# Kernel optimization log

Measured on AMD Instinct MI355X. Metric: run time of the kernel, lower is better.

The kernel has to match this reference:

```python
import math
import jax, jax.numpy as jnp
from jax import lax
import numpy as np

C, H, W, N, K = 256, 64, 64, 16, 7

def setup_inputs() -> dict:
    key = jax.random.key(0)
    k0, k1, k2, k3, k4 = jax.random.split(key, 5)
    x = jax.random.normal(k0, (N, C, H, W), dtype=jnp.float32)
    p_2_w = 0.02 * jax.random.normal(k1, (1, C, H, 1), dtype=jnp.float32)
    # nn.Conv2d(c, c, (1,5), groups=1, bias=False) -> weight [c, c, 1, 5]
    fan_in = C * 1 * 5
    bound = 1.0 / math.sqrt(fan_in)
    p_3_w = jax.random.uniform(k2, (C, C, 1, 5), dtype=jnp.float32, minval=-bound, maxval=bound)
    p_4_w = 0.02 * jax.random.normal(k3, (1, C, K, 1, 1), dtype=jnp.float32)
    p_6_w = jax.random.uniform(k4, (K, 1), dtype=jnp.float32, minval=-7.0, maxval=7.0)
    return {"x": x, "p_2_w": p_2_w, "p_3_w": p_3_w, "p_4_w": p_4_w, "p_6_w": p_6_w}

def reference(x, p_2_w, p_3_w, p_4_w, p_6_w):
    n, c, h, w = x.shape
    k = p_4_w.shape[2]  # 7 taps
    pad = (k - 1) // 2
    # F.unfold with kernel (1,7), pad (0,3): stack 7 width-shifted copies -> [n,c,7,h,w]
    xp = jnp.pad(x, ((0, 0), (0, 0), (0, 0), (pad, pad)))
    t_1 = jnp.stack([xp[..., i:i + w] for i in range(k)], axis=2)
    # per-(channel,row) scaling then dense 1x5 conv
    t_2 = p_2_w * x
    t_3 = lax.conv_general_dilated(
        t_2, p_3_w, window_strides=(1, 1), padding=[(0, 0), (2, 2)],
        dimension_numbers=("NCHW", "OIHW", "NCHW"))
    # weighted tap-sum: (p_4_w * t_1) contracted over taps with p_6_w[:,0]
    t_4 = p_4_w * t_1
    t_6 = jnp.einsum("nckhw,kf->ncfhw", t_4, p_6_w)[:, :, 0]  # [n,c,h,w]
    t_5 = jax.nn.relu(x)
    s = h * w
    # channel-attention matrix [n,c,c]
    t_7 = jnp.einsum("ncs,nds->ncd", t_3.reshape(n, c, s), t_6.reshape(n, c, s))
    t_7 = t_7 * (1.0 / math.sqrt(s))
    # bmm(t_5^T, t_7) -> [n,s,d]; permuting to [n,d,h,w] == einsum 'ncs,ncd->nds'
    out = jnp.einsum("ncs,ncd->nds", t_5.reshape(n, c, s), t_7)
    out = out * (1.0 / math.sqrt(c))
    return out.reshape(n, c, h, w)
```

## Files before the change

kernel.cpp:

```cpp
#include <hip/hip_runtime.h>
#include <hip/hip_bf16.h>

typedef __attribute__((ext_vector_type(8))) short bf16x8;
typedef __attribute__((ext_vector_type(4))) float f32x4;

#define NB 16
#define CD 256
#define HD 64
#define WD 64
#define WP 68
#define SD 4096
#define KU 1280

__device__ __forceinline__ void gload16(const void* g, void* lds) {
  __builtin_amdgcn_global_load_lds(
      (const __attribute__((address_space(1))) unsigned int*)g,
      (__attribute__((address_space(3))) unsigned int*)lds, 16, 0, 0);
}

__global__ __launch_bounds__(256) void prep_x(const float* __restrict__ x,
                                              const float* __restrict__ p2,
                                              const float* __restrict__ p4,
                                              const float* __restrict__ p6,
                                              const float* __restrict__ p3,
                                              __hip_bfloat16* __restrict__ t2p,
                                              __hip_bfloat16* __restrict__ t5T,
                                              __hip_bfloat16* __restrict__ t6,
                                              __hip_bfloat16* __restrict__ A) {
  int h = blockIdx.x;
  int cb = blockIdx.y;
  int n = blockIdx.z;
  int c0 = cb * 64;
  __shared__ float xwp[64][72];
  __shared__ __hip_bfloat16 t5l[64][72];
  __shared__ __hip_bfloat16 t2l[64][72];
  int t = threadIdx.x;

  {
    int bid = (n * 64 + h) * 4 + cb;
    int id = bid * 256 + t;
    if (id < CD * KU) {
      int o = id / KU;
      int r = id - o * KU;
      int j = r >> 8;
      int c = r & 255;
      A[id] = __float2bfloat16(p3[(o * CD + c) * 5 + j]);
    }
  }

  {
    int r = t >> 2, cc = t & 3;
    xwp[r][cc] = 0.f;
    xwp[r][68 + cc] = 0.f;
  }

  {
    int w = t & 63, cg = (t >> 6) * 16;
    __hip_bfloat16 o5[16], o2[16];
#pragma unroll
    for (int j = 0; j < 16; ++j) {
      int c = c0 + cg + j;
      float xv = x[(((size_t)n * CD + c) * HD + h) * WD + w];
      float sc = p2[c * HD + h];
      xwp[cg + j][4 + w] = xv;
      o5[j] = __float2bfloat16(fmaxf(xv, 0.f));
      o2[j] = __float2bfloat16(sc * xv);
    }
    *reinterpret_cast<bf16x8*>(&t5l[w][cg]) = *reinterpret_cast<const bf16x8*>(&o5[0]);
    *reinterpret_cast<bf16x8*>(&t5l[w][cg + 8]) = *reinterpret_cast<const bf16x8*>(&o5[8]);
    *reinterpret_cast<bf16x8*>(&t2l[w][cg]) = *reinterpret_cast<const bf16x8*>(&o2[0]);
    *reinterpret_cast<bf16x8*>(&t2l[w][cg + 8]) = *reinterpret_cast<const bf16x8*>(&o2[8]);
  }
  __syncthreads();

  __hip_bfloat16* t2pn = t2p + (size_t)n * HD * WP * CD;

  {
    int ws = t >> 2, ch = (t & 3) * 16;
    bf16x8 v0 = *reinterpret_cast<const bf16x8*>(&t5l[ws][ch]);
    bf16x8 v1 = *reinterpret_cast<const bf16x8*>(&t5l[ws][ch + 8]);
    size_t s = (size_t)h * 64 + ws;
    *reinterpret_cast<bf16x8*>(&t5T[((size_t)n * SD + s) * CD + c0 + ch]) = v0;
    *reinterpret_cast<bf16x8*>(&t5T[((size_t)n * SD + s) * CD + c0 + ch + 8]) = v1;
    bf16x8 u0 = *reinterpret_cast<const bf16x8*>(&t2l[ws][ch]);
    bf16x8 u1 = *reinterpret_cast<const bf16x8*>(&t2l[ws][ch + 8]);
    *reinterpret_cast<bf16x8*>(&t2pn[((size_t)h * WP + ws + 2) * CD + c0 + ch]) = u0;
    *reinterpret_cast<bf16x8*>(&t2pn[((size_t)h * WP + ws + 2) * CD + c0 + ch + 8]) = u1;
  }
  if (t < 32) {
    int pi = t >> 3;
    int wp = (pi < 2) ? pi : pi + 64;
    int cc = (t & 7) * 8;
    bf16x8 z = (bf16x8){0, 0, 0, 0, 0, 0, 0, 0};
    *reinterpret_cast<bf16x8*>(&t2pn[((size_t)h * WP + wp) * CD + c0 + cc]) = z;
  }

  {
    int cl = t >> 2, w16 = (t & 3) * 16;
    float hx[24];
#pragma unroll
    for (int q = 0; q < 6; ++q) {
      float4 v = *reinterpret_cast<const float4*>(&xwp[cl][w16 + q * 4]);
      hx[q * 4 + 0] = v.x;
      hx[q * 4 + 1] = v.y;
      hx[q * 4 + 2] = v.z;
      hx[q * 4 + 3] = v.w;
    }
    float wt[7];
#pragma unroll
    for (int k = 0; k < 7; ++k) wt[k] = p4[(c0 + cl) * 7 + k] * p6[k];
    __hip_bfloat16 o6[16];
#pragma unroll
    for (int u = 0; u < 16; ++u) {
      float acc = 0.f;
#pragma unroll
      for (int k = 0; k < 7; ++k) acc += wt[k] * hx[u + 1 + k];
      o6[u] = __float2bfloat16(acc);
    }
    size_t base = ((size_t)n * CD + c0 + cl) * SD + h * 64 + w16;
    *reinterpret_cast<bf16x8*>(&t6[base]) = *reinterpret_cast<const bf16x8*>(&o6[0]);
    *reinterpret_cast<bf16x8*>(&t6[base + 8]) = *reinterpret_cast<const bf16x8*>(&o6[8]);
  }
}

#define VMWAIT(N) asm volatile("s_waitcnt vmcnt(" #N ")" ::: "memory")
#define BARRIER() __builtin_amdgcn_s_barrier()

#define ST4(kt, bi)                                                                    \
  do {                                                                                 \
    char* dst = lb + ((bi) << 15) + t * 16;                                            \
    gload16(gA0 + (kt) * 64, dst);                                                     \
    gload16(gA1 + (kt) * 64, dst + 8192);                                              \
    gload16(gB0 + (kt) * 64, dst + 16384);                                             \
    gload16(gB1 + (kt) * 64, dst + 24576);                                             \
  } while (0)

#define LDF(bi, AV, BV)                                                                \
  do {                                                                                 \
    const char* ba = lb + ((bi) << 15);                                                \
    _Pragma("unroll") for (int mf = 0; mf < 8; ++mf) {                                 \
      int row = wm * 128 + mf * 16 + l16;                                              \
      AV[mf] = *reinterpret_cast<const bf16x8*>(ba + row * 64 + ((lg ^ rxor) * 16));   \
    }                                                                                  \
    _Pragma("unroll") for (int nf = 0; nf < 4; ++nf) {                                 \
      int row = wn * 64 + nf * 16 + l16;                                               \
      BV[nf] = *reinterpret_cast<const bf16x8*>(ba + 16384 + row * 64 +                \
                                                ((lg ^ rxor) * 16));                   \
    }                                                                                  \
  } while (0)

#define MM(AV, BV)                                                                     \
  do {                                                                                 \
    __builtin_amdgcn_s_setprio(1);                                                     \
    _Pragma("unroll") for (int mf = 0; mf < 8; ++mf)                                   \
        _Pragma("unroll") for (int nf = 0; nf < 4; ++nf)                               \
            acc[mf][nf] = __builtin_amdgcn_mfma_f32_16x16x32_bf16(AV[mf], BV[nf],      \
                                                                  acc[mf][nf], 0, 0, 0); \
    __builtin_amdgcn_s_setprio(0);                                                     \
  } while (0)

__global__ __launch_bounds__(512, 2) void gemm_b8(const __hip_bfloat16* __restrict__ A,
                                                  const __hip_bfloat16* __restrict__ t2p,
                                                  __hip_bfloat16* __restrict__ t3) {
  __shared__ __align__(16) __hip_bfloat16 lds[65536];
  char* lb = (char*)lds;
  const int n = blockIdx.z;
  const int sb = blockIdx.x;
  const int t = threadIdx.x;
  const int wv = t >> 6, lane = t & 63;
  const int wm = wv >> 2, wn = wv & 3;
  const int l16 = lane & 15, lg = lane >> 4;
  const int s0 = sb * 256;
  const int rxor = (l16 >> 1) & 3;
  const char* Ab = (const char*)A;
  const char* t2pb = (const char*)(t2p + (size_t)n * HD * WP * CD);
  const int cbsrc = ((t & 3) ^ ((t >> 3) & 3)) * 16;

  const int r0 = t >> 2;
  const char* gA0 = Ab + (size_t)r0 * 2560 + cbsrc;
  const char* gA1 = Ab + (size_t)(r0 + 128) * 2560 + cbsrc;
  const int s1 = s0 + r0, s2 = s0 + r0 + 128;
  const char* gB0 = t2pb + (size_t)(s1 + 4 * (s1 >> 6)) * 512 + cbsrc;
  const char* gB1 = t2pb + (size_t)(s2 + 4 * (s2 >> 6)) * 512 + cbsrc;

  f32x4 acc[8][4];
#pragma unroll
  for (int i = 0; i < 8; ++i)
#pragma unroll
    for (int j = 0; j < 4; ++j) acc[i][j] = (f32x4){0.f, 0.f, 0.f, 0.f};

  bf16x8 avX[8], bvX[4], avY[8], bvY[4];

  ST4(0, 0);
  ST4(1, 1);
  VMWAIT(4);
  BARRIER();
  LDF(0, avX, bvX);

  for (int k2 = 0; k2 < 18; ++k2) {
    const int kt = k2 * 2;
    ST4(kt + 2, (kt + 2) & 3);
    MM(avX, bvX);
    VMWAIT(4);
    BARRIER();
    LDF((kt + 1) & 3, avY, bvY);
    ST4(kt + 3, (kt + 3) & 3);
    MM(avY, bvY);
    VMWAIT(4);
    BARRIER();
    LDF((kt + 2) & 3, avX, bvX);
  }
  ST4(38, 2);
  MM(avX, bvX);
  VMWAIT(4);
  BARRIER();
  LDF(1, avY, bvY);
  ST4(39, 3);
  MM(avY, bvY);
  VMWAIT(4);
  BARRIER();
  LDF(2, avX, bvX);
  MM(avX, bvX);
  VMWAIT(0);
  BARRIER();
  LDF(3, avY, bvY);
  MM(avY, bvY);

  __hip_bfloat16* t3n = t3 + (size_t)n * CD * SD;
#pragma unroll
  for (int im = 0; im < 8; ++im)
#pragma unroll
    for (int in = 0; in < 4; ++in) {
      int row0 = wm * 128 + im * 16 + lg * 4;
      int col = s0 + wn * 64 + in * 16 + l16;
#pragma unroll
      for (int r = 0; r < 4; ++r)
        t3n[(size_t)(row0 + r) * SD + col] = __float2bfloat16(acc[im][in][r]);
    }
}

__global__ __launch_bounds__(256) void gemm_c_part(const __hip_bfloat16* __restrict__ t6,
                                                   const __hip_bfloat16* __restrict__ t3,
                                                   float* __restrict__ P4) {
  __shared__ __align__(16) __hip_bfloat16 lA[64 * 64];
  __shared__ __align__(16) __hip_bfloat16 lB[64 * 64];
  int bx = blockIdx.x;
  int cbk = bx & 3, kc = bx >> 2;
  int db = blockIdx.y;
  int n = blockIdx.z;
  int t = threadIdx.x;
  int wave = t >> 6, lane = t & 63;
  int wm = wave >> 1, wn = wave & 1;
  int l16 = lane & 15, lg = lane >> 4;
  int d0 = db * 64;
  int c0 = cbk * 64;
  int kbase = kc * 1024;
  const __hip_bfloat16* An = t6 + (size_t)n * CD * SD + kbase;
  const __hip_bfloat16* Bn = t3 + (size_t)n * CD * SD + kbase;

  int srow = t >> 3;
  int scol = (t & 7) * 8;
  const __hip_bfloat16* gA0 = An + (size_t)(d0 + srow) * SD + scol;
  const __hip_bfloat16* gA1 = An + (size_t)(d0 + srow + 32) * SD + scol;
  const __hip_bfloat16* gB0 = Bn + (size_t)(c0 + srow) * SD + scol;
  const __hip_bfloat16* gB1 = Bn + (size_t)(c0 + srow + 32) * SD + scol;
  __hip_bfloat16* lAd0 = &lA[t * 8];
  __hip_bfloat16* lAd1 = &lA[t * 8 + 32 * 64];
  __hip_bfloat16* lBd0 = &lB[t * 8];
  __hip_bfloat16* lBd1 = &lB[t * 8 + 32 * 64];

  f32x4 acc[2][2];
#pragma unroll
  for (int mi = 0; mi < 2; ++mi)
#pragma unroll
    for (int ni = 0; ni < 2; ++ni) acc[mi][ni] = (f32x4){0.f, 0.f, 0.f, 0.f};

  gload16(gA0, lAd0);
  gload16(gA1, lAd1);
  gload16(gB0, lBd0);
  gload16(gB1, lBd1);

  for (int k = 0; k < 16; ++k) {
    __syncthreads();
#pragma unroll
    for (int ks = 0; ks < 2; ++ks) {
      bf16x8 a[2], b[2];
#pragma unroll
      for (int mi = 0; mi < 2; ++mi)
        a[mi] = *reinterpret_cast<const bf16x8*>(&lA[(wm * 32 + mi * 16 + l16) * 64 + ks * 32 + lg * 8]);
#pragma unroll
      for (int ni = 0; ni < 2; ++ni)
        b[ni] = *reinterpret_cast<const bf16x8*>(&lB[(wn * 32 + ni * 16 + l16) * 64 + ks * 32 + lg * 8]);
#pragma unroll
      for (int mi = 0; mi < 2; ++mi)
#pragma unroll
        for (int ni = 0; ni < 2; ++ni)
          acc[mi][ni] = __builtin_amdgcn_mfma_f32_16x16x32_bf16(a[mi], b[ni], acc[mi][ni], 0, 0, 0);
    }
    __syncthreads();
    if (k < 15) {
      int kk = (k + 1) * 64;
      gload16(gA0 + kk, lAd0);
      gload16(gA1 + kk, lAd1);
      gload16(gB0 + kk, lBd0);
      gload16(gB1 + kk, lBd1);
    }
  }

  float* Pn = P4 + ((size_t)kc * NB + n) * CD * CD;
#pragma unroll
  for (int mi = 0; mi < 2; ++mi)
#pragma unroll
    for (int ni = 0; ni < 2; ++ni) {
      int col = c0 + wn * 32 + ni * 16 + l16;
      int row0 = d0 + wm * 32 + mi * 16 + lg * 4;
#pragma unroll
      for (int r = 0; r < 4; ++r)
        Pn[(size_t)(row0 + r) * CD + col] = acc[mi][ni][r];
    }
}

__global__ __launch_bounds__(256) void reduce_P(const float* __restrict__ P4,
                                                __hip_bfloat16* __restrict__ P) {
  size_t i = ((size_t)blockIdx.x * 256 + threadIdx.x) * 4;
  const size_t stride = (size_t)NB * CD * CD;
  float4 a = *reinterpret_cast<const float4*>(P4 + i);
  float4 b = *reinterpret_cast<const float4*>(P4 + stride + i);
  float4 c = *reinterpret_cast<const float4*>(P4 + 2 * stride + i);
  float4 d = *reinterpret_cast<const float4*>(P4 + 3 * stride + i);
  __hip_bfloat16 o[4];
  o[0] = __float2bfloat16((a.x + b.x + c.x + d.x) * 0.015625f);
  o[1] = __float2bfloat16((a.y + b.y + c.y + d.y) * 0.015625f);
  o[2] = __float2bfloat16((a.z + b.z + c.z + d.z) * 0.015625f);
  o[3] = __float2bfloat16((a.w + b.w + c.w + d.w) * 0.015625f);
  *reinterpret_cast<short4*>(&P[i]) = *reinterpret_cast<const short4*>(o);
}

#define DSTAGE_A(i, kk)                                                                \
  gload16(Pb + (size_t)((i) * 32 + wv4 * 8 + (lane >> 3)) * 512 + (kk) * 128 + cbsrc,  \
          (char*)lA + (i) * 4096 + wv4 * 1024)
#define DSTAGE_B(i, kk)                                                                \
  gload16(Tb + (size_t)(s0 + (i) * 32 + wv4 * 8 + (lane >> 3)) * 512 + (kk) * 128 + cbsrc, \
          (char*)lB + (i) * 4096 + wv4 * 1024)

__global__ __launch_bounds__(256, 2) void gemm_d(const __hip_bfloat16* __restrict__ P,
                                                 const __hip_bfloat16* __restrict__ t5T,
                                                 float* __restrict__ out) {
  __shared__ __align__(16) __hip_bfloat16 lA[256 * 64];
  __shared__ __align__(16) __hip_bfloat16 lB[128 * 64];
  const int n = blockIdx.z;
  const int sb = blockIdx.x;
  const int t = threadIdx.x;
  const int wv4 = t >> 6, lane = t & 63;
  const int wm = wv4 >> 1, wn = wv4 & 1;
  const int l16 = lane & 15, lg = lane >> 4;
  const int s0 = sb * 128;
  const char* Pb = (const char*)(P + (size_t)n * CD * CD);
  const char* Tb = (const char*)(t5T + (size_t)n * SD * CD);
  const int cbsrc = ((lane & 7) ^ (lane >> 3)) * 16;
  const int lxor = (l16 & 7) * 8;

  f32x4 acc[8][4];
#pragma unroll
  for (int i = 0; i < 8; ++i)
#pragma unroll
    for (int j = 0; j < 4; ++j) acc[i][j] = (f32x4){0.f, 0.f, 0.f, 0.f};

#pragma unroll
  for (int i = 0; i < 8; ++i) DSTAGE_A(i, 0);
#pragma unroll
  for (int i = 0; i < 4; ++i) DSTAGE_B(i, 0);

  for (int k = 0; k < 4; ++k) {
    __syncthreads();
#pragma unroll
    for (int ks = 0; ks < 2; ++ks) {
      int cb = (ks * 32 + lg * 8) ^ lxor;
      bf16x8 a[8], b[4];
#pragma unroll
      for (int mf = 0; mf < 8; ++mf)
        a[mf] = *reinterpret_cast<const bf16x8*>(&lA[(wm * 128 + mf * 16 + l16) * 64 + cb]);
#pragma unroll
      for (int nf = 0; nf < 4; ++nf)
        b[nf] = *reinterpret_cast<const bf16x8*>(&lB[(wn * 64 + nf * 16 + l16) * 64 + cb]);
#pragma unroll
      for (int mf = 0; mf < 8; ++mf)
#pragma unroll
        for (int nf = 0; nf < 4; ++nf)
          acc[mf][nf] = __builtin_amdgcn_mfma_f32_16x16x32_bf16(a[mf], b[nf], acc[mf][nf], 0, 0, 0);
    }
    __syncthreads();
    if (k < 3) {
      int kk = k + 1;
#pragma unroll
      for (int i = 0; i < 8; ++i) DSTAGE_A(i, kk);
#pragma unroll
      for (int i = 0; i < 4; ++i) DSTAGE_B(i, kk);
    }
  }

  float* outn = out + (size_t)n * CD * SD;
#pragma unroll
  for (int mf = 0; mf < 8; ++mf)
#pragma unroll
    for (int nf = 0; nf < 4; ++nf) {
      int col = s0 + wn * 64 + nf * 16 + l16;
      int row0 = wm * 128 + mf * 16 + lg * 4;
#pragma unroll
      for (int r = 0; r < 4; ++r)
        outn[(size_t)(row0 + r) * SD + col] = acc[mf][nf][r] * 0.0625f;
    }
}

extern "C" void kernel_launch(void* const* d_in, const int* in_sizes, int n_in,
                              void* d_out, int out_size, void* d_ws, size_t ws_size,
                              hipStream_t stream) {
  const float* x = (const float*)d_in[0];
  const float* p2 = (const float*)d_in[1];
  const float* p3 = (const float*)d_in[2];
  const float* p4 = (const float*)d_in[3];
  const float* p6 = (const float*)d_in[4];

  char* ws = (char*)d_ws;
  size_t off = 0;
  __hip_bfloat16* A = (__hip_bfloat16*)(ws + off);
  off += (size_t)CD * KU * 2;
  size_t t2p_off = off;
  __hip_bfloat16* t2p = (__hip_bfloat16*)(ws + off);
  off += (size_t)NB * HD * WP * CD * 2;
  __hip_bfloat16* t5T = (__hip_bfloat16*)(ws + off);
  off += (size_t)NB * SD * CD * 2;
  __hip_bfloat16* t6 = (__hip_bfloat16*)(ws + off);
  off += (size_t)NB * CD * SD * 2;
  __hip_bfloat16* t3 = (__hip_bfloat16*)(ws + off);
  off += (size_t)NB * CD * SD * 2;
  float* P4 = (float*)(ws + t2p_off);
  __hip_bfloat16* P = (__hip_bfloat16*)(ws + t2p_off + (size_t)4 * NB * CD * CD * 4);

  float* out = (float*)d_out;

  prep_x<<<dim3(HD, 4, NB), 256, 0, stream>>>(x, p2, p4, p6, p3, t2p, t5T, t6, A);
  gemm_b8<<<dim3(16, 1, NB), 512, 0, stream>>>(A, t2p, t3);
  gemm_c_part<<<dim3(16, 4, NB), 256, 0, stream>>>(t6, t3, P4);
  reduce_P<<<dim3((NB * CD * CD / 4) / 256), 256, 0, stream>>>(P4, P);
  gemm_d<<<dim3(32, 1, NB), 256, 0, stream>>>(P, t5T, out);
}
```

Measured before the change: 130.6 us.

## Fuse split-K partial reduction into gemm_d A-tile staging and remap block order

The separate reduce_P kernel is removed. gemm_d now loads the four fp32 split-K partials directly, sums and scales them, converts to bf16 and writes the A tile into LDS, saving one launch and the intermediate bf16 round trip. Both gemm_c_part and gemm_d also remap the flat block index so that blocks likely to share data or run on the same XCD are grouped, and prep_x's LDS row pitch is padded to reduce bank conflicts. In exchange, each gemm_d block redundantly re-reads and re-reduces the full 256x256 P partials for its batch, which multiplies fp32 traffic across the 32 s-blocks. The synchronous A loads also replace the asynchronous LDS loads for that operand.

```diff
diff --git a/kernel.cpp b/kernel.cpp
--- a/kernel.cpp
+++ b/kernel.cpp
@@ -31,7 +31,7 @@
   int cb = blockIdx.y;
   int n = blockIdx.z;
   int c0 = cb * 64;
-  __shared__ float xwp[64][72];
+  __shared__ float xwp[64][76];
   __shared__ __hip_bfloat16 t5l[64][72];
   __shared__ __hip_bfloat16 t2l[64][72];
   int t = threadIdx.x;
@@ -244,10 +244,11 @@
                                                    float* __restrict__ P4) {
   __shared__ __align__(16) __hip_bfloat16 lA[64 * 64];
   __shared__ __align__(16) __hip_bfloat16 lB[64 * 64];
-  int bx = blockIdx.x;
-  int cbk = bx & 3, kc = bx >> 2;
-  int db = blockIdx.y;
-  int n = blockIdx.z;
+  int flat = blockIdx.x + 16 * blockIdx.y + 64 * blockIdx.z;
+  int lgid = (flat & 7) * 128 + (flat >> 3);
+  int cbk = lgid & 3, kc = (lgid >> 2) & 3;
+  int db = (lgid >> 4) & 3;
+  int n = lgid >> 6;
   int t = threadIdx.x;
   int wave = t >> 6, lane = t & 63;
   int wm = wave >> 1, wn = wave & 1;
@@ -320,44 +321,53 @@
     }
 }
 
-__global__ __launch_bounds__(256) void reduce_P(const float* __restrict__ P4,
-                                                __hip_bfloat16* __restrict__ P) {
-  size_t i = ((size_t)blockIdx.x * 256 + threadIdx.x) * 4;
-  const size_t stride = (size_t)NB * CD * CD;
-  float4 a = *reinterpret_cast<const float4*>(P4 + i);
-  float4 b = *reinterpret_cast<const float4*>(P4 + stride + i);
-  float4 c = *reinterpret_cast<const float4*>(P4 + 2 * stride + i);
-  float4 d = *reinterpret_cast<const float4*>(P4 + 3 * stride + i);
-  __hip_bfloat16 o[4];
-  o[0] = __float2bfloat16((a.x + b.x + c.x + d.x) * 0.015625f);
-  o[1] = __float2bfloat16((a.y + b.y + c.y + d.y) * 0.015625f);
-  o[2] = __float2bfloat16((a.z + b.z + c.z + d.z) * 0.015625f);
-  o[3] = __float2bfloat16((a.w + b.w + c.w + d.w) * 0.015625f);
-  *reinterpret_cast<short4*>(&P[i]) = *reinterpret_cast<const short4*>(o);
-}
-
+#define NBCC ((size_t)NB * CD * CD)
 #define DSTAGE_A(i, kk)                                                                \
-  gload16(Pb + (size_t)((i) * 32 + wv4 * 8 + (lane >> 3)) * 512 + (kk) * 128 + cbsrc,  \
-          (char*)lA + (i) * 4096 + wv4 * 1024)
+  do {                                                                                 \
+    int r_ = (i) * 32 + wv4 * 8 + (lane >> 3);                                         \
+    const float* p_ = P4n + (size_t)r_ * CD + (kk) * 64 + gsrc8;                       \
+    float4 a0 = *reinterpret_cast<const float4*>(p_);                                  \
+    float4 a1 = *reinterpret_cast<const float4*>(p_ + 4);                              \
+    float4 b0 = *reinterpret_cast<const float4*>(p_ + NBCC);                           \
+    float4 b1 = *reinterpret_cast<const float4*>(p_ + NBCC + 4);                       \
+    float4 c0 = *reinterpret_cast<const float4*>(p_ + 2 * NBCC);                       \
+    float4 c1 = *reinterpret_cast<const float4*>(p_ + 2 * NBCC + 4);                   \
+    float4 d0 = *reinterpret_cast<const float4*>(p_ + 3 * NBCC);                       \
+    float4 d1 = *reinterpret_cast<const float4*>(p_ + 3 * NBCC + 4);                   \
+    __hip_bfloat16 o_[8];                                                              \
+    o_[0] = __float2bfloat16((a0.x + b0.x + c0.x + d0.x) * 0.015625f);                 \
+    o_[1] = __float2bfloat16((a0.y + b0.y + c0.y + d0.y) * 0.015625f);                 \
+    o_[2] = __float2bfloat16((a0.z + b0.z + c0.z + d0.z) * 0.015625f);                 \
+    o_[3] = __float2bfloat16((a0.w + b0.w + c0.w + d0.w) * 0.015625f);                 \
+    o_[4] = __float2bfloat16((a1.x + b1.x + c1.x + d1.x) * 0.015625f);                 \
+    o_[5] = __float2bfloat16((a1.y + b1.y + c1.y + d1.y) * 0.015625f);                 \
+    o_[6] = __float2bfloat16((a1.z + b1.z + c1.z + d1.z) * 0.015625f);                 \
+    o_[7] = __float2bfloat16((a1.w + b1.w + c1.w + d1.w) * 0.015625f);                 \
+    *reinterpret_cast<bf16x8*>((char*)lA + r_ * 128 + (lane & 7) * 16) =               \
+        *reinterpret_cast<const bf16x8*>(o_);                                          \
+  } while (0)
 #define DSTAGE_B(i, kk)                                                                \
   gload16(Tb + (size_t)(s0 + (i) * 32 + wv4 * 8 + (lane >> 3)) * 512 + (kk) * 128 + cbsrc, \
           (char*)lB + (i) * 4096 + wv4 * 1024)
 
-__global__ __launch_bounds__(256, 2) void gemm_d(const __hip_bfloat16* __restrict__ P,
+__global__ __launch_bounds__(256, 2) void gemm_d(const float* __restrict__ P4,
                                                  const __hip_bfloat16* __restrict__ t5T,
                                                  float* __restrict__ out) {
   __shared__ __align__(16) __hip_bfloat16 lA[256 * 64];
   __shared__ __align__(16) __hip_bfloat16 lB[128 * 64];
-  const int n = blockIdx.z;
-  const int sb = blockIdx.x;
+  int flat = blockIdx.x + 32 * blockIdx.z;
+  int lgid = (flat & 7) * 64 + (flat >> 3);
+  const int sb = lgid & 31;
+  const int n = lgid >> 5;
   const int t = threadIdx.x;
   const int wv4 = t >> 6, lane = t & 63;
   const int wm = wv4 >> 1, wn = wv4 & 1;
   const int l16 = lane & 15, lg = lane >> 4;
   const int s0 = sb * 128;
-  const char* Pb = (const char*)(P + (size_t)n * CD * CD);
+  const float* P4n = P4 + (size_t)n * CD * CD;
   const char* Tb = (const char*)(t5T + (size_t)n * SD * CD);
   const int cbsrc = ((lane & 7) ^ (lane >> 3)) * 16;
+  const int gsrc8 = ((lane & 7) ^ (lane >> 3)) * 8;
   const int lxor = (l16 & 7) * 8;
 
   f32x4 acc[8][4];
@@ -435,13 +445,11 @@
   __hip_bfloat16* t3 = (__hip_bfloat16*)(ws + off);
   off += (size_t)NB * CD * SD * 2;
   float* P4 = (float*)(ws + t2p_off);
-  __hip_bfloat16* P = (__hip_bfloat16*)(ws + t2p_off + (size_t)4 * NB * CD * CD * 4);
 
   float* out = (float*)d_out;
 
   prep_x<<<dim3(HD, 4, NB), 256, 0, stream>>>(x, p2, p4, p6, p3, t2p, t5T, t6, A);
   gemm_b8<<<dim3(16, 1, NB), 512, 0, stream>>>(A, t2p, t3);
   gemm_c_part<<<dim3(16, 4, NB), 256, 0, stream>>>(t6, t3, P4);
-  reduce_P<<<dim3((NB * CD * CD / 4) / 256), 256, 0, stream>>>(P4, P);
-  gemm_d<<<dim3(32, 1, NB), 256, 0, stream>>>(P, t5T, out);
-}
+  gemm_d<<<dim3(32, 1, NB), 256, 0, stream>>>(P4, t5T, out);
+}
```

New measurement: 137.0 us. 1.05x slower.
